# Kernel optimization log

Measured on AMD Instinct MI355X. Metric: run time of the kernel, lower is better.

The kernel has to match this reference:

```python
import jax, jax.numpy as jnp
import numpy as np
from jax.scipy.linalg import expm

B, HW, SPP, C, H, W = 4, 16384, 3, 64, 128, 128
D_SH = 25
EPS = 1e-8

# color SH mask: higher degrees downweighted (from GaussianAdapter.__init__)
_SH_MASK = np.ones(D_SH, np.float32)
for _d in range(1, 5):
    _SH_MASK[_d * _d:(_d + 1) * (_d + 1)] = 0.1 * 0.25 ** _d

# --- e3nn-style SO(3) generators for wigner_D (precomputed in numpy) ---

def _su2_generators(j):
    m = np.arange(-j, j)
    raising = np.diag(-np.sqrt(j * (j + 1) - m * (m + 1)), k=-1).astype(np.complex128)
    m = np.arange(-j + 1, j + 1)
    lowering = np.diag(np.sqrt(j * (j + 1) - m * (m - 1)), k=1).astype(np.complex128)
    m = np.arange(-j, j + 1)
    return np.stack([0.5 * (raising + lowering), np.diag(1j * m), -0.5j * (raising - lowering)])

def _change_basis(l):
    q = np.zeros((2 * l + 1, 2 * l + 1), dtype=np.complex128)
    for m in range(-l, 0):
        q[l + m, l + abs(m)] = 1 / np.sqrt(2)
        q[l + m, l - abs(m)] = -1j / np.sqrt(2)
    q[l, l] = 1.0
    for m in range(1, l + 1):
        q[l + m, l + abs(m)] = (-1) ** m / np.sqrt(2)
        q[l + m, l - abs(m)] = 1j * (-1) ** m / np.sqrt(2)
    return (-1j) ** l * q

def _so3_generators(l):
    X = _su2_generators(l)
    Q = _change_basis(l)
    return np.real(np.conj(Q.T) @ X @ Q).astype(np.float32)

_SO3 = [_so3_generators(l) for l in range(5)]

# --- small math helpers ---

def _quat_to_mat(q):  # q: (..., 4) wxyz, pytorch3d convention
    r, i, j, k = q[..., 0], q[..., 1], q[..., 2], q[..., 3]
    s = 2.0 / jnp.sum(q * q, axis=-1)
    m = jnp.stack([
        1 - s * (j * j + k * k), s * (i * j - k * r), s * (i * k + j * r),
        s * (i * j + k * r), 1 - s * (i * i + k * k), s * (j * k - i * r),
        s * (i * k - j * r), s * (j * k + i * r), 1 - s * (i * i + j * j)], -1)
    return m.reshape(q.shape[:-1] + (3, 3))

def _rot_y(a):
    c, s = jnp.cos(a), jnp.sin(a)
    z, o = jnp.zeros_like(a), jnp.ones_like(a)
    return jnp.stack([jnp.stack([c, z, s], -1), jnp.stack([z, o, z], -1), jnp.stack([-s, z, c], -1)], -2)

def _rot_x(a):
    c, s = jnp.cos(a), jnp.sin(a)
    z, o = jnp.zeros_like(a), jnp.ones_like(a)
    return jnp.stack([jnp.stack([o, z, z], -1), jnp.stack([z, c, -s], -1), jnp.stack([z, s, c], -1)], -2)

def _matrix_to_angles(R):  # e3nn matrix_to_angles, YXY convention
    x = R[..., :, 1]  # R @ e_y
    x = x / jnp.linalg.norm(x, axis=-1, keepdims=True)
    beta = jnp.arccos(jnp.clip(x[..., 1], -1.0, 1.0))
    alpha = jnp.arctan2(x[..., 0], x[..., 2])
    A = _rot_y(alpha) @ _rot_x(beta)  # angles_to_matrix(alpha, beta, 0)
    Rp = jnp.swapaxes(A, -1, -2) @ R
    gamma = jnp.arctan2(Rp[..., 0, 2], Rp[..., 0, 0])
    return alpha, beta, gamma

def _wigner_D(l, alpha, beta, gamma):  # alpha/beta/gamma: [b]
    X = jnp.asarray(_SO3[l])
    ea = jax.vmap(expm)(alpha[:, None, None] * X[1])
    eb = jax.vmap(expm)(beta[:, None, None] * X[0])
    eg = jax.vmap(expm)(gamma[:, None, None] * X[1])
    return ea @ eb @ eg  # [b, 2l+1, 2l+1]

def _rotate_sh(sh, R):  # sh: [b,hw,spp,3,25], R: [b,3,3]
    alpha, beta, gamma = _matrix_to_angles(R)
    out = []
    for l in range(5):
        D = _wigner_D(l, alpha, -beta, gamma)
        out.append(jnp.einsum('bij,bhscj->bhsci', D, sh[..., l * l:(l + 1) * (l + 1)]))
    return jnp.concatenate(out, axis=-1)

def _forward(extrinsics, intrinsics, coordinates, depths, opacities, raw_gaussians, grd_feat, image_h, image_w):
    scales_raw = raw_gaussians[..., :3]
    rot_raw = raw_gaussians[..., 3:7]
    color_sh = raw_gaussians[..., 7:7 + 3 * D_SH]
    b, c, h, w = grd_feat.shape
    features = jnp.transpose(grd_feat.reshape(b, c, h * w), (0, 2, 1))[:, :, None, :]  # [b,hw,1,c]
    scales = 0.5 + (15.0 - 0.5) * jax.nn.sigmoid(scales_raw)
    pixel_size = jnp.array([1.0 / image_w, 1.0 / image_h], dtype=jnp.float32)
    K2inv = jnp.linalg.inv(intrinsics[..., :2, :2])
    multiplier = 0.1 * jnp.einsum('bij,j->bi', K2inv, pixel_size).sum(-1)  # [b]
    scales = scales * depths[..., None] * multiplier[:, None, None, None]
    rotations = rot_raw / (jnp.linalg.norm(rot_raw, axis=-1, keepdims=True) + EPS)
    color_sh = color_sh.reshape(color_sh.shape[:-1] + (3, D_SH)) * jnp.asarray(_SH_MASK)
    features = jnp.broadcast_to(features, opacities.shape + (c,))
    # covariance = R S S^T R^T
    Rq = _quat_to_mat(rotations)
    covariances = jnp.einsum('...ij,...j,...kj->...ik', Rq, scales * scales, Rq)
    # world rays
    Kinv = jnp.linalg.inv(intrinsics)
    coords_h = jnp.concatenate([coordinates, jnp.ones_like(coordinates[..., :1])], -1)
    dirs = jnp.einsum('bij,bhsj->bhsi', Kinv, coords_h)
    dirs = dirs / jnp.linalg.norm(dirs, axis=-1, keepdims=True)
    Rc2w = extrinsics[..., :3, :3]
    dirs = jnp.einsum('bij,bhsj->bhsi', Rc2w, dirs)
    origins = extrinsics[:, None, None, :3, 3]
    means = origins + dirs * depths[..., None]
    sh_rot = _rotate_sh(color_sh, Rc2w)
    rotations = jnp.broadcast_to(rotations, scales.shape[:-1] + (4,))
    return (means, covariances, sh_rot, opacities, features, scales, rotations)

def setup_inputs() -> dict:
    key = jax.random.key(0)
    ks = jax.random.split(key, 8)
    q = jax.random.normal(ks[0], (B, 4), jnp.float32)
    q = q / jnp.linalg.norm(q, axis=-1, keepdims=True)
    R = _quat_to_mat(q)
    t = jax.random.normal(ks[1], (B, 3), jnp.float32)
    extrinsics = jnp.tile(jnp.eye(4, dtype=jnp.float32), (B, 1, 1)).at[:, :3, :3].set(R).at[:, :3, 3].set(t)
    f = jax.random.uniform(ks[2], (B, 2), jnp.float32, 0.4, 0.6)
    intrinsics = (jnp.zeros((B, 3, 3), jnp.float32)
                  .at[:, 0, 0].set(f[:, 0]).at[:, 1, 1].set(f[:, 1])
                  .at[:, 0, 2].set(0.5).at[:, 1, 2].set(0.5).at[:, 2, 2].set(1.0))
    coordinates = jax.random.uniform(ks[3], (B, HW, SPP, 2), jnp.float32)
    depths = jax.random.uniform(ks[4], (B, HW, SPP), jnp.float32) * 50.0 + 0.5
    opacities = jax.random.uniform(ks[5], (B, HW, SPP), jnp.float32)
    raw_gaussians = jax.random.normal(ks[6], (B, HW, SPP, 3 + 4 + 3 * D_SH), jnp.float32)
    grd_feat = jax.random.normal(ks[7], (B, C, H, W), jnp.float32)
    return {"extrinsics": extrinsics, "intrinsics": intrinsics, "coordinates": coordinates,
            "depths": depths, "opacities": opacities, "raw_gaussians": raw_gaussians,
            "grd_feat": grd_feat, "image_h": H, "image_w": W}

def reference(extrinsics, intrinsics, coordinates, depths, opacities, raw_gaussians, grd_feat, image_h, image_w):
    return _forward(extrinsics, intrinsics, coordinates, depths, opacities, raw_gaussians, grd_feat, image_h, image_w)
```

## Files before the change

### kernel.cpp

```cpp
#include <hip/hip_runtime.h>
#include <math.h>

#define N_TOT   196608
#define HWSPP   49152
#define RGF     82
#define RGS     83

#define OFF_MEANS 0
#define OFF_COV   589824
#define OFF_SH    2359296
#define OFF_OP    17104896
#define OFF_FEAT  17301504
#define OFF_SCL   29884416
#define OFF_ROT   30474240

__device__ __constant__ int c_loff[5] = {0, 1, 10, 35, 84};

__device__ __forceinline__ float sigmoidf_(float x) { return 1.0f / (1.0f + expf(-x)); }

__global__ __launch_bounds__(256) void setup_kernel(
    const float* __restrict__ extr, const float* __restrict__ intr,
    const int* __restrict__ img_h, const int* __restrict__ img_w,
    float* __restrict__ ws)
{
  const int b = blockIdx.x / 5;
  const int l = blockIdx.x % 5;
  const int n = 2 * l + 1;
  const int nn = n * n;
  const int t = threadIdx.x;

  __shared__ double Qr[81], Qi[81], X0c[81], Trr[81], Tii[81], X0r[81], X1r[81];
  __shared__ double GA[3][81], GP[3][81], GT[3][81], OUT3[3][81], M1[81];
  __shared__ double ang[3];
  __shared__ int s3[3];
  __shared__ int smax;

  if (t == 0) {
    const float* E = extr + b * 16;
    double R00 = E[0], R01 = E[1], R02 = E[2];
    double R11 = E[5];
    double R20 = E[8], R21 = E[9], R22 = E[10];
    double x0 = R01, x1 = R11, x2 = R21;
    double nr = sqrt(x0 * x0 + x1 * x1 + x2 * x2);
    x0 /= nr; x1 /= nr; x2 /= nr;
    double beta  = acos(fmin(1.0, fmax(-1.0, x1)));
    double alpha = atan2(x0, x2);
    double ca = cos(alpha), sa = sin(alpha);
    double gamma = atan2(ca * R02 - sa * R22, ca * R00 - sa * R20);
    ang[0] = alpha; ang[1] = beta; ang[2] = gamma;
    if (l == 0) {
      const float* K = intr + b * 9;
      double k00=K[0],k01=K[1],k02=K[2],k10=K[3],k11=K[4],k12=K[5],k20=K[6],k21=K[7],k22=K[8];
      double det = k00*(k11*k22-k12*k21) - k01*(k10*k22-k12*k20) + k02*(k10*k21-k11*k20);
      double id = 1.0 / det;
      float* kv = ws + 660 + b * 9;
      kv[0] = (float)((k11*k22-k12*k21)*id);
      kv[1] = (float)((k02*k21-k01*k22)*id);
      kv[2] = (float)((k01*k12-k02*k11)*id);
      kv[3] = (float)((k12*k20-k10*k22)*id);
      kv[4] = (float)((k00*k22-k02*k20)*id);
      kv[5] = (float)((k02*k10-k00*k12)*id);
      kv[6] = (float)((k10*k21-k11*k20)*id);
      kv[7] = (float)((k01*k20-k00*k21)*id);
      kv[8] = (float)((k00*k11-k01*k10)*id);
      double d2 = k00 * k11 - k01 * k10;
      double ps0 = 1.0 / (double)img_w[0];
      double ps1 = 1.0 / (double)img_h[0];
      double sum = (k11 * ps0 - k01 * ps1 - k10 * ps0 + k00 * ps1) / d2;
      ws[696 + b] = (float)(0.1 * sum);
    }
  }
  if (t < 81) { Qr[t] = 0.0; Qi[t] = 0.0; X0c[t] = 0.0; }
  __syncthreads();
  if (t == 0) {
    const double irt2 = 0.70710678118654752440;
    for (int m = -l; m < 0; ++m) {
      Qr[(l + m) * n + (l - m)] = irt2;
      Qi[(l + m) * n + (l + m)] = -irt2;
    }
    Qr[l * n + l] = 1.0;
    for (int m = 1; m <= l; ++m) {
      double sg = (m & 1) ? -1.0 : 1.0;
      Qr[(l + m) * n + (l + m)] = sg * irt2;
      Qi[(l + m) * n + (l - m)] = sg * irt2;
    }
    for (int i = 0; i < n - 1; ++i) {
      double mi = (double)(-l + i);
      double ci = sqrt((double)(l * (l + 1)) - mi * (mi + 1.0));
      X0c[i * n + (i + 1)] = 0.5 * ci;
      X0c[(i + 1) * n + i] = -0.5 * ci;
    }
  }
  __syncthreads();
  if (t < nn) {
    int i = t / n, j = t % n; double s = 0, s2 = 0;
    for (int k = 0; k < n; ++k) { s += X0c[i*n+k]*Qr[k*n+j]; s2 += X0c[i*n+k]*Qi[k*n+j]; }
    Trr[t] = s; Tii[t] = s2;
  }
  __syncthreads();
  if (t < nn) {
    int a = t / n, c = t % n; double s = 0, s1 = 0;
    for (int r = 0; r < n; ++r) {
      s  += Qr[r*n+a]*Trr[r*n+c] + Qi[r*n+a]*Tii[r*n+c];
      double mr = (double)(r - l);
      s1 += mr * (Qi[r*n+a]*Qr[r*n+c] - Qr[r*n+a]*Qi[r*n+c]);
    }
    X0r[t] = s; X1r[t] = s1;
  }
  __syncthreads();

  const int g  = t / 81;
  const int gt = t - g * 81;
  if (t < 243 && gt == 0) {
    const double* X = (g == 1) ? X0r : X1r;
    double th = (g == 0) ? ang[0] : ((g == 1) ? -ang[1] : ang[2]);
    double mx = 0.0;
    for (int i = 0; i < n; ++i) {
      double rs = 0.0;
      for (int j = 0; j < n; ++j) rs += fabs(th * X[i * n + j]);
      mx = fmax(mx, rs);
    }
    int s = 0;
    while (mx > 0.25) { mx *= 0.5; ++s; }
    s3[g] = s;
  }
  __syncthreads();
  if (t == 0) smax = max(s3[0], max(s3[1], s3[2]));
  __syncthreads();
  if (t < 243 && gt < nn) {
    const double* X = (g == 1) ? X0r : X1r;
    double th = (g == 0) ? ang[0] : ((g == 1) ? -ang[1] : ang[2]);
    for (int q = 0; q < s3[g]; ++q) th *= 0.5;
    GA[g][gt] = th * X[gt];
    GP[g][gt] = GA[g][gt];
    OUT3[g][gt] = ((gt / n) == (gt % n) ? 1.0 : 0.0) + GA[g][gt];
  }
  __syncthreads();
  for (int k = 2; k <= 14; ++k) {
    if (t < 243 && gt < nn) {
      int i = gt / n, j = gt % n; double s = 0;
      for (int kk = 0; kk < n; ++kk) s += GP[g][i*n+kk] * GA[g][kk*n+j];
      GT[g][gt] = s;
    }
    __syncthreads();
    if (t < 243 && gt < nn) { GP[g][gt] = GT[g][gt] / (double)k; OUT3[g][gt] += GP[g][gt]; }
    __syncthreads();
  }
  for (int q = 0; q < smax; ++q) {
    if (t < 243 && gt < nn) {
      if (q < s3[g]) {
        int i = gt / n, j = gt % n; double s = 0;
        for (int kk = 0; kk < n; ++kk) s += OUT3[g][i*n+kk] * OUT3[g][kk*n+j];
        GT[g][gt] = s;
      } else GT[g][gt] = OUT3[g][gt];
    }
    __syncthreads();
    if (t < 243 && gt < nn) OUT3[g][gt] = GT[g][gt];
    __syncthreads();
  }
  if (t < nn) {
    int i = t / n, j = t % n; double s = 0;
    for (int k = 0; k < n; ++k) s += OUT3[0][i*n+k] * OUT3[1][k*n+j];
    M1[t] = s;
  }
  __syncthreads();
  if (t < nn) {
    int i = t / n, j = t % n; double s = 0;
    for (int k = 0; k < n; ++k) s += M1[i*n+k] * OUT3[2][k*n+j];
    ws[b * 165 + c_loff[l] + t] = (float)s;
  }
}

__global__ __launch_bounds__(256) void gauss_kernel(
    const float* __restrict__ extr,
    const float* __restrict__ coords,
    const float* __restrict__ depths,
    const float* __restrict__ opac,
    const float* __restrict__ rg,
    const float* __restrict__ ws,
    float* __restrict__ out)
{
  __shared__ float sIn[64 * RGS];
  __shared__ __align__(16) float sSh[64 * 75];
  __shared__ float sSmall[1280];
  __shared__ float sD[165];
  __shared__ float sKinv[9], sRc[9], sOrig[3];
  __shared__ float sMult;

  const int t  = threadIdx.x;
  const int g0 = blockIdx.x * 64;
  const int b  = g0 / HWSPP;

  if (t < 165) sD[t] = ws[b * 165 + t];
  else if (t < 174) sKinv[t - 165] = ws[660 + b * 9 + (t - 165)];
  else if (t < 183) { int k = t - 174; sRc[k] = extr[b * 16 + (k / 3) * 4 + (k % 3)]; }
  else if (t < 186) sOrig[t - 183] = extr[b * 16 + (t - 183) * 4 + 3];
  else if (t == 186) sMult = ws[696 + b];

  {
    const float4* src4 = (const float4*)(rg + (size_t)g0 * RGF);
    for (int idx = t; idx < (64 * RGF) / 4; idx += 256) {
      float4 v = src4[idx];
      int base = idx * 4;
      int gg = base / RGF;
      int ff = base - gg * RGF;
      float vv[4] = {v.x, v.y, v.z, v.w};
#pragma unroll
      for (int e = 0; e < 4; ++e) {
        int g2 = gg, f2 = ff + e;
        if (f2 >= RGF) { g2 += 1; f2 -= RGF; }
        sIn[g2 * RGS + f2] = vv[e];
      }
    }
  }
  __syncthreads();

  if (t < 64) {
    const int gidx = g0 + t;
    const float* q = &sIn[t * RGS];
    const float dpt = depths[gidx];
    const float mlt = sMult;
    float sc0 = (0.5f + 14.5f * sigmoidf_(q[0])) * dpt * mlt;
    float sc1 = (0.5f + 14.5f * sigmoidf_(q[1])) * dpt * mlt;
    float sc2 = (0.5f + 14.5f * sigmoidf_(q[2])) * dpt * mlt;
    float r0 = q[3], r1 = q[4], r2 = q[5], r3 = q[6];
    float nr = sqrtf(r0*r0 + r1*r1 + r2*r2 + r3*r3) + 1e-8f;
    float qr = r0/nr, qi = r1/nr, qj = r2/nr, qk = r3/nr;
    float s2 = 2.0f / (qr*qr + qi*qi + qj*qj + qk*qk);
    float R00 = 1.0f - s2*(qj*qj + qk*qk);
    float R01 = s2*(qi*qj - qk*qr);
    float R02 = s2*(qi*qk + qj*qr);
    float R10 = s2*(qi*qj + qk*qr);
    float R11 = 1.0f - s2*(qi*qi + qk*qk);
    float R12 = s2*(qj*qk - qi*qr);
    float R20 = s2*(qi*qk - qj*qr);
    float R21 = s2*(qj*qk + qi*qr);
    float R22 = 1.0f - s2*(qi*qi + qj*qj);
    float v0 = sc0*sc0, v1 = sc1*sc1, v2 = sc2*sc2;
    float C00 = R00*R00*v0 + R01*R01*v1 + R02*R02*v2;
    float C01 = R00*R10*v0 + R01*R11*v1 + R02*R12*v2;
    float C02 = R00*R20*v0 + R01*R21*v1 + R02*R22*v2;
    float C11 = R10*R10*v0 + R11*R11*v1 + R12*R12*v2;
    float C12 = R10*R20*v0 + R11*R21*v1 + R12*R22*v2;
    float C22 = R20*R20*v0 + R21*R21*v1 + R22*R22*v2;
    float2 cxy = ((const float2*)coords)[gidx];
    float dx = sKinv[0]*cxy.x + sKinv[1]*cxy.y + sKinv[2];
    float dy = sKinv[3]*cxy.x + sKinv[4]*cxy.y + sKinv[5];
    float dz = sKinv[6]*cxy.x + sKinv[7]*cxy.y + sKinv[8];
    float inr = 1.0f / sqrtf(dx*dx + dy*dy + dz*dz);
    dx *= inr; dy *= inr; dz *= inr;
    float wx = sRc[0]*dx + sRc[1]*dy + sRc[2]*dz;
    float wy = sRc[3]*dx + sRc[4]*dy + sRc[5]*dz;
    float wz = sRc[6]*dx + sRc[7]*dy + sRc[8]*dz;
    sSmall[t*3+0] = sOrig[0] + wx * dpt;
    sSmall[t*3+1] = sOrig[1] + wy * dpt;
    sSmall[t*3+2] = sOrig[2] + wz * dpt;
    float* cc = &sSmall[192 + t*9];
    cc[0]=C00; cc[1]=C01; cc[2]=C02; cc[3]=C01; cc[4]=C11; cc[5]=C12; cc[6]=C02; cc[7]=C12; cc[8]=C22;
    float* ss = &sSmall[768 + t*3]; ss[0]=sc0; ss[1]=sc1; ss[2]=sc2;
    float* rr = &sSmall[960 + t*4]; rr[0]=qr; rr[1]=qi; rr[2]=qj; rr[3]=qk;
    sSmall[1216 + t] = opac[gidx];
  } else {
    const int task = t - 64;
    const int gg = task & 63;
    const int ch = task >> 6;
    const float* shin = &sIn[gg * RGS + 7 + ch * 25];
    float* shout = &sSh[gg * 75 + ch * 25];
    float in_[25];
#pragma unroll
    for (int j = 0; j < 25; ++j) in_[j] = shin[j];
    shout[0] = sD[0] * in_[0];
#pragma unroll
    for (int i = 0; i < 3; ++i) {
      float a = sD[1+i*3]*in_[1] + sD[1+i*3+1]*in_[2] + sD[1+i*3+2]*in_[3];
      shout[1 + i] = (float)(0.1 * 0.25) * a;
    }
#pragma unroll
    for (int i = 0; i < 5; ++i) {
      float a = 0.f;
#pragma unroll
      for (int j = 0; j < 5; ++j) a += sD[10 + i*5 + j] * in_[4 + j];
      shout[4 + i] = (float)(0.1 * 0.0625) * a;
    }
#pragma unroll
    for (int i = 0; i < 7; ++i) {
      float a = 0.f;
#pragma unroll
      for (int j = 0; j < 7; ++j) a += sD[35 + i*7 + j] * in_[9 + j];
      shout[9 + i] = (float)(0.1 * 0.015625) * a;
    }
#pragma unroll
    for (int i = 0; i < 9; ++i) {
      float a = 0.f;
#pragma unroll
      for (int j = 0; j < 9; ++j) a += sD[84 + i*9 + j] * in_[16 + j];
      shout[16 + i] = (float)(0.1 * 0.00390625) * a;
    }
  }
  __syncthreads();

  {
    float4* osh = (float4*)(out + OFF_SH + (size_t)g0 * 75);
    const float4* s4 = (const float4*)sSh;
    for (int idx = t; idx < 1200; idx += 256) osh[idx] = s4[idx];
    float* om  = out + OFF_MEANS + (size_t)g0 * 3;
    float* oc  = out + OFF_COV   + (size_t)g0 * 9;
    float* os  = out + OFF_SCL   + (size_t)g0 * 3;
    float* orr = out + OFF_ROT   + (size_t)g0 * 4;
    float* oo  = out + OFF_OP    + (size_t)g0;
    if (t < 192) { om[t] = sSmall[t]; os[t] = sSmall[768 + t]; }
    for (int idx = t; idx < 576; idx += 256) oc[idx] = sSmall[192 + idx];
    orr[t] = sSmall[960 + t];
    if (t < 64) oo[t] = sSmall[1216 + t];
  }
}

__global__ __launch_bounds__(256) void feat_kernel(
    const float* __restrict__ gf, float* __restrict__ out)
{
  __shared__ float tile[64 * 65];
  const int t = threadIdx.x;
  const int blk = blockIdx.x;
  const int b = blk >> 8;
  const int hw0 = (blk & 255) << 6;
  const int tx = t & 63, ty = t >> 6;
  const float* src = gf + (size_t)b * 64 * 16384 + hw0;
#pragma unroll
  for (int i = 0; i < 16; ++i) {
    int c = i * 4 + ty;
    tile[c * 65 + tx] = src[(size_t)c * 16384 + tx];
  }
  __syncthreads();
  float* dst = out + OFF_FEAT + ((size_t)(b * 16384 + hw0)) * 3 * 64;
  for (int r = ty; r < 192; r += 4) {
    int hw = r / 3;
    dst[(size_t)r * 64 + tx] = tile[tx * 65 + hw];
  }
}

extern "C" void kernel_launch(void* const* d_in, const int* in_sizes, int n_in,
                              void* d_out, int out_size, void* d_ws, size_t ws_size,
                              hipStream_t stream)
{
  const float* extr   = (const float*)d_in[0];
  const float* intr   = (const float*)d_in[1];
  const float* coords = (const float*)d_in[2];
  const float* depths = (const float*)d_in[3];
  const float* opac   = (const float*)d_in[4];
  const float* rg     = (const float*)d_in[5];
  const float* gf     = (const float*)d_in[6];
  const int*   ih     = (const int*)d_in[7];
  const int*   iw     = (const int*)d_in[8];
  float* out = (float*)d_out;
  float* ws  = (float*)d_ws;

  hipLaunchKernelGGL(setup_kernel, dim3(20), dim3(256), 0, stream, extr, intr, ih, iw, ws);
  hipLaunchKernelGGL(gauss_kernel, dim3(N_TOT / 64), dim3(256), 0, stream,
                     extr, coords, depths, opac, rg, ws, out);
  hipLaunchKernelGGL(feat_kernel, dim3(1024), dim3(256), 0, stream, gf, out);
}
```

Measured before the change: 240.4 us.

## Merge feature transpose into gaussian kernel and shrink setup to one wavefront

Merges the feature-map transpose kernel into the gaussian kernel as extra blocks with a shared-memory union, removing one launch and letting both workloads run on the GPU at the same time. The setup kernel now uses 64 threads and processes the three exponentials one after another instead of in parallel, with less shared memory. The trade-off is a serial setup with more barrier rounds, and the merged kernel's shared-memory footprint is set by the larger gaussian path, which may limit occupancy for the transpose blocks.

New measurement: 287.7 us. 19.7% more time.

```diff
diff --git a/kernel.cpp b/kernel.cpp
--- a/kernel.cpp
+++ b/kernel.cpp
@@ -5,6 +5,8 @@
 #define HWSPP   49152
 #define RGF     82
 #define RGS     83
+#define NGB     3072
+#define NFB     1024
 
 #define OFF_MEANS 0
 #define OFF_COV   589824
@@ -18,7 +20,7 @@
 
 __device__ __forceinline__ float sigmoidf_(float x) { return 1.0f / (1.0f + expf(-x)); }
 
-__global__ __launch_bounds__(256) void setup_kernel(
+__global__ __launch_bounds__(64) void setup_kernel(
     const float* __restrict__ extr, const float* __restrict__ intr,
     const int* __restrict__ img_h, const int* __restrict__ img_w,
     float* __restrict__ ws)
@@ -29,17 +31,16 @@
   const int nn = n * n;
   const int t = threadIdx.x;
 
-  __shared__ double Qr[81], Qi[81], X0c[81], Trr[81], Tii[81], X0r[81], X1r[81];
-  __shared__ double GA[3][81], GP[3][81], GT[3][81], OUT3[3][81], M1[81];
+  __shared__ double Qr[81], Qi[81], X0c[81], X0r[81], X1r[81];
+  __shared__ double E[3][81], A_[81], P_[81], T_[81], M1[81];
   __shared__ double ang[3];
-  __shared__ int s3[3];
-  __shared__ int smax;
+  __shared__ int sS;
 
   if (t == 0) {
-    const float* E = extr + b * 16;
-    double R00 = E[0], R01 = E[1], R02 = E[2];
-    double R11 = E[5];
-    double R20 = E[8], R21 = E[9], R22 = E[10];
+    const float* Ex = extr + b * 16;
+    double R00 = Ex[0], R01 = Ex[1], R02 = Ex[2];
+    double R11 = Ex[5];
+    double R20 = Ex[8], R21 = Ex[9], R22 = Ex[10];
     double x0 = R01, x1 = R11, x2 = R21;
     double nr = sqrt(x0 * x0 + x1 * x1 + x2 * x2);
     x0 /= nr; x1 /= nr; x2 /= nr;
@@ -70,7 +71,7 @@
       ws[696 + b] = (float)(0.1 * sum);
     }
   }
-  if (t < 81) { Qr[t] = 0.0; Qi[t] = 0.0; X0c[t] = 0.0; }
+  for (int e = t; e < 81; e += 64) { Qr[e] = 0.0; Qi[e] = 0.0; X0c[e] = 0.0; }
   __syncthreads();
   if (t == 0) {
     const double irt2 = 0.70710678118654752440;
@@ -92,102 +93,124 @@
     }
   }
   __syncthreads();
-  if (t < nn) {
-    int i = t / n, j = t % n; double s = 0, s2 = 0;
+  for (int e = t; e < nn; e += 64) {
+    int i = e / n, j = e % n; double s = 0, s2 = 0;
     for (int k = 0; k < n; ++k) { s += X0c[i*n+k]*Qr[k*n+j]; s2 += X0c[i*n+k]*Qi[k*n+j]; }
-    Trr[t] = s; Tii[t] = s2;
-  }
-  __syncthreads();
-  if (t < nn) {
-    int a = t / n, c = t % n; double s = 0, s1 = 0;
+    A_[e] = s; P_[e] = s2;
+  }
+  __syncthreads();
+  for (int e = t; e < nn; e += 64) {
+    int a = e / n, c = e % n; double s = 0, s1 = 0;
     for (int r = 0; r < n; ++r) {
-      s  += Qr[r*n+a]*Trr[r*n+c] + Qi[r*n+a]*Tii[r*n+c];
+      s  += Qr[r*n+a]*A_[r*n+c] + Qi[r*n+a]*P_[r*n+c];
       double mr = (double)(r - l);
       s1 += mr * (Qi[r*n+a]*Qr[r*n+c] - Qr[r*n+a]*Qi[r*n+c]);
     }
-    X0r[t] = s; X1r[t] = s1;
-  }
-  __syncthreads();
-
-  const int g  = t / 81;
-  const int gt = t - g * 81;
-  if (t < 243 && gt == 0) {
+    X0r[e] = s; X1r[e] = s1;
+  }
+  __syncthreads();
+
+  for (int g = 0; g < 3; ++g) {
     const double* X = (g == 1) ? X0r : X1r;
     double th = (g == 0) ? ang[0] : ((g == 1) ? -ang[1] : ang[2]);
-    double mx = 0.0;
-    for (int i = 0; i < n; ++i) {
-      double rs = 0.0;
-      for (int j = 0; j < n; ++j) rs += fabs(th * X[i * n + j]);
-      mx = fmax(mx, rs);
-    }
-    int s = 0;
-    while (mx > 0.25) { mx *= 0.5; ++s; }
-    s3[g] = s;
-  }
-  __syncthreads();
-  if (t == 0) smax = max(s3[0], max(s3[1], s3[2]));
-  __syncthreads();
-  if (t < 243 && gt < nn) {
-    const double* X = (g == 1) ? X0r : X1r;
-    double th = (g == 0) ? ang[0] : ((g == 1) ? -ang[1] : ang[2]);
-    for (int q = 0; q < s3[g]; ++q) th *= 0.5;
-    GA[g][gt] = th * X[gt];
-    GP[g][gt] = GA[g][gt];
-    OUT3[g][gt] = ((gt / n) == (gt % n) ? 1.0 : 0.0) + GA[g][gt];
-  }
-  __syncthreads();
-  for (int k = 2; k <= 14; ++k) {
-    if (t < 243 && gt < nn) {
-      int i = gt / n, j = gt % n; double s = 0;
-      for (int kk = 0; kk < n; ++kk) s += GP[g][i*n+kk] * GA[g][kk*n+j];
-      GT[g][gt] = s;
+    if (t == 0) {
+      double mx = 0.0;
+      for (int i = 0; i < n; ++i) {
+        double rs = 0.0;
+        for (int j = 0; j < n; ++j) rs += fabs(th * X[i * n + j]);
+        mx = fmax(mx, rs);
+      }
+      int s = 0;
+      while (mx > 0.25) { mx *= 0.5; ++s; }
+      sS = s;
     }
     __syncthreads();
-    if (t < 243 && gt < nn) { GP[g][gt] = GT[g][gt] / (double)k; OUT3[g][gt] += GP[g][gt]; }
+    const int sq = sS;
+    double ths = th;
+    for (int q = 0; q < sq; ++q) ths *= 0.5;
+    for (int e = t; e < nn; e += 64) {
+      A_[e] = ths * X[e];
+      P_[e] = A_[e];
+      E[g][e] = ((e / n) == (e % n) ? 1.0 : 0.0) + A_[e];
+    }
     __syncthreads();
-  }
-  for (int q = 0; q < smax; ++q) {
-    if (t < 243 && gt < nn) {
-      if (q < s3[g]) {
-        int i = gt / n, j = gt % n; double s = 0;
-        for (int kk = 0; kk < n; ++kk) s += OUT3[g][i*n+kk] * OUT3[g][kk*n+j];
-        GT[g][gt] = s;
-      } else GT[g][gt] = OUT3[g][gt];
-    }
-    __syncthreads();
-    if (t < 243 && gt < nn) OUT3[g][gt] = GT[g][gt];
-    __syncthreads();
-  }
-  if (t < nn) {
-    int i = t / n, j = t % n; double s = 0;
-    for (int k = 0; k < n; ++k) s += OUT3[0][i*n+k] * OUT3[1][k*n+j];
-    M1[t] = s;
-  }
-  __syncthreads();
-  if (t < nn) {
-    int i = t / n, j = t % n; double s = 0;
-    for (int k = 0; k < n; ++k) s += M1[i*n+k] * OUT3[2][k*n+j];
-    ws[b * 165 + c_loff[l] + t] = (float)s;
+    for (int k = 2; k <= 14; ++k) {
+      for (int e = t; e < nn; e += 64) {
+        int i = e / n, j = e % n; double s = 0;
+        for (int kk = 0; kk < n; ++kk) s += P_[i*n+kk] * A_[kk*n+j];
+        T_[e] = s;
+      }
+      __syncthreads();
+      for (int e = t; e < nn; e += 64) { P_[e] = T_[e] / (double)k; E[g][e] += P_[e]; }
+      __syncthreads();
+    }
+    for (int q = 0; q < sq; ++q) {
+      for (int e = t; e < nn; e += 64) {
+        int i = e / n, j = e % n; double s = 0;
+        for (int kk = 0; kk < n; ++kk) s += E[g][i*n+kk] * E[g][kk*n+j];
+        T_[e] = s;
+      }
+      __syncthreads();
+      for (int e = t; e < nn; e += 64) E[g][e] = T_[e];
+      __syncthreads();
+    }
+  }
+  for (int e = t; e < nn; e += 64) {
+    int i = e / n, j = e % n; double s = 0;
+    for (int k = 0; k < n; ++k) s += E[0][i*n+k] * E[1][k*n+j];
+    M1[e] = s;
+  }
+  __syncthreads();
+  for (int e = t; e < nn; e += 64) {
+    int i = e / n, j = e % n; double s = 0;
+    for (int k = 0; k < n; ++k) s += M1[i*n+k] * E[2][k*n+j];
+    ws[b * 165 + c_loff[l] + e] = (float)s;
   }
 }
 
-__global__ __launch_bounds__(256) void gauss_kernel(
+__global__ __launch_bounds__(256) void main_kernel(
     const float* __restrict__ extr,
     const float* __restrict__ coords,
     const float* __restrict__ depths,
     const float* __restrict__ opac,
     const float* __restrict__ rg,
+    const float* __restrict__ gf,
     const float* __restrict__ ws,
     float* __restrict__ out)
 {
-  __shared__ float sIn[64 * RGS];
-  __shared__ __align__(16) float sSh[64 * 75];
-  __shared__ float sSmall[1280];
-  __shared__ float sD[165];
-  __shared__ float sKinv[9], sRc[9], sOrig[3];
-  __shared__ float sMult;
-
-  const int t  = threadIdx.x;
+  __shared__ __align__(16) float smem[11584];
+  const int t = threadIdx.x;
+
+  if (blockIdx.x >= NGB) {
+    float* tile = smem;
+    const int blk = blockIdx.x - NGB;
+    const int b = blk >> 8;
+    const int hw0 = (blk & 255) << 6;
+    const int tx = t & 63, ty = t >> 6;
+    const float* src = gf + (size_t)b * 64 * 16384 + hw0;
+#pragma unroll
+    for (int i = 0; i < 16; ++i) {
+      int c = i * 4 + ty;
+      tile[c * 65 + tx] = src[(size_t)c * 16384 + tx];
+    }
+    __syncthreads();
+    float* dst = out + OFF_FEAT + ((size_t)(b * 16384 + hw0)) * 3 * 64;
+    for (int r = ty; r < 192; r += 4) {
+      int hw = r / 3;
+      dst[(size_t)r * 64 + tx] = tile[tx * 65 + hw];
+    }
+    return;
+  }
+
+  float* sIn    = smem;
+  float* sSh    = smem + 5312;
+  float* sSmall = smem + 10112;
+  float* sD     = smem + 11392;
+  float* sKinv  = smem + 11557;
+  float* sRc    = smem + 11566;
+  float* sOrig  = smem + 11575;
+  float* sMult  = smem + 11578;
+
   const int g0 = blockIdx.x * 64;
   const int b  = g0 / HWSPP;
 
@@ -195,7 +218,7 @@
   else if (t < 174) sKinv[t - 165] = ws[660 + b * 9 + (t - 165)];
   else if (t < 183) { int k = t - 174; sRc[k] = extr[b * 16 + (k / 3) * 4 + (k % 3)]; }
   else if (t < 186) sOrig[t - 183] = extr[b * 16 + (t - 183) * 4 + 3];
-  else if (t == 186) sMult = ws[696 + b];
+  else if (t == 186) sMult[0] = ws[696 + b];
 
   {
     const float4* src4 = (const float4*)(rg + (size_t)g0 * RGF);
@@ -219,7 +242,7 @@
     const int gidx = g0 + t;
     const float* q = &sIn[t * RGS];
     const float dpt = depths[gidx];
-    const float mlt = sMult;
+    const float mlt = sMult[0];
     float sc0 = (0.5f + 14.5f * sigmoidf_(q[0])) * dpt * mlt;
     float sc1 = (0.5f + 14.5f * sigmoidf_(q[1])) * dpt * mlt;
     float sc2 = (0.5f + 14.5f * sigmoidf_(q[2])) * dpt * mlt;
@@ -315,29 +338,6 @@
   }
 }
 
-__global__ __launch_bounds__(256) void feat_kernel(
-    const float* __restrict__ gf, float* __restrict__ out)
-{
-  __shared__ float tile[64 * 65];
-  const int t = threadIdx.x;
-  const int blk = blockIdx.x;
-  const int b = blk >> 8;
-  const int hw0 = (blk & 255) << 6;
-  const int tx = t & 63, ty = t >> 6;
-  const float* src = gf + (size_t)b * 64 * 16384 + hw0;
-#pragma unroll
-  for (int i = 0; i < 16; ++i) {
-    int c = i * 4 + ty;
-    tile[c * 65 + tx] = src[(size_t)c * 16384 + tx];
-  }
-  __syncthreads();
-  float* dst = out + OFF_FEAT + ((size_t)(b * 16384 + hw0)) * 3 * 64;
-  for (int r = ty; r < 192; r += 4) {
-    int hw = r / 3;
-    dst[(size_t)r * 64 + tx] = tile[tx * 65 + hw];
-  }
-}
-
 extern "C" void kernel_launch(void* const* d_in, const int* in_sizes, int n_in,
                               void* d_out, int out_size, void* d_ws, size_t ws_size,
                               hipStream_t stream)
@@ -354,8 +354,7 @@
   float* out = (float*)d_out;
   float* ws  = (float*)d_ws;
 
-  hipLaunchKernelGGL(setup_kernel, dim3(20), dim3(256), 0, stream, extr, intr, ih, iw, ws);
-  hipLaunchKernelGGL(gauss_kernel, dim3(N_TOT / 64), dim3(256), 0, stream,
-                     extr, coords, depths, opac, rg, ws, out);
-  hipLaunchKernelGGL(feat_kernel, dim3(1024), dim3(256), 0, stream, gf, out);
+  hipLaunchKernelGGL(setup_kernel, dim3(20), dim3(64), 0, stream, extr, intr, ih, iw, ws);
+  hipLaunchKernelGGL(main_kernel, dim3(NGB + NFB), dim3(256), 0, stream,
+                     extr, coords, depths, opac, rg, gf, ws, out);
 }
```
